# Performance work log

Hardware: AMD Instinct MI355X
Metric: run time of the kernel (lower is better)

## Reference

```python
import jax, jax.numpy as jnp
import numpy as np
import math

# ---- static configuration (matches init_kwargs) ----
B = 2
CIN, COUT = 128, 128
NLAT_IN, NLON_IN = 181, 360
NLAT_OUT, NLON_OUT = 181, 360
KSIZE = 3
PSCALE = NLON_IN // NLON_OUT  # longitude stride between output shifts
THETA_CUTOFF = KSIZE * math.pi / float(NLAT_IN - 1)


def _cc_weights(n):
    """Clenshaw-Curtis quadrature weights on [-1,1] for n equiangular nodes."""
    N = n - 1
    tk = np.pi * np.arange(n) / N
    j = np.arange(1, N // 2 + 1)
    b = np.where(2 * j == N, 1.0, 2.0)
    s = (b / (4.0 * j * j - 1.0)) @ np.cos(2.0 * np.outer(j, tk))
    w = (2.0 / N) * (1.0 - s)
    w[0] *= 0.5
    w[-1] *= 0.5
    return w[::-1].copy()  # flipped, as in _precompute_latitudes


def _lats(n):
    tk = np.pi * np.arange(n) / (n - 1)
    return tk[::-1].copy()  # lats = flip(arccos(cos(theta_k)))


def _precompute_psi():
    """Replicates _precompute_convolution_tensor + _compute_support_vals_isotropic.
    Returns COO entries (seg = k*NLAT_OUT + t, lat_in, lon_in, val)."""
    lats_in = _lats(NLAT_IN)
    lats_out = _lats(NLAT_OUT)
    phis = np.linspace(0.0, 2.0 * np.pi, NLON_IN)  # endpoint included (torch.linspace)
    dtheta = THETA_CUTOFF / KSIZE
    norm = 2.0 * np.pi * (1.0 - np.cos(THETA_CUTOFF))
    segs, lat_idx, lon_idx, vals = [], [], [], []
    alpha = lats_in[:, None]           # (nlat_in, 1)
    beta = phis[None, :]               # (1, nlon_in)
    for t in range(NLAT_OUT):
        gamma = lats_out[t]
        z = np.cos(alpha) * np.cos(gamma) - np.cos(beta) * np.sin(alpha) * np.sin(gamma)
        theta = np.arccos(np.clip(z, -1.0, 1.0))  # geodesic distance to rotated pole
        for k in range(KSIZE):
            d = np.abs(theta - k * dtheta)
            mask = (d <= dtheta) & (theta <= THETA_CUTOFF)
            ii, jj = np.nonzero(mask)
            if ii.size == 0:
                continue
            segs.append(np.full(ii.size, k * NLAT_OUT + t, dtype=np.int32))
            lat_idx.append(ii.astype(np.int32))
            lon_idx.append(jj.astype(np.int32))
            vals.append(((1.0 - d[ii, jj] / dtheta) / norm).astype(np.float32))
    return (np.concatenate(segs), np.concatenate(lat_idx),
            np.concatenate(lon_idx), np.concatenate(vals))


def setup_inputs() -> dict:
    key = jax.random.key(0)
    k1, k2, k3 = jax.random.split(key, 3)
    x = jax.random.normal(k1, (B, CIN, NLAT_IN, NLON_IN), dtype=jnp.float32)
    wgl = _cc_weights(NLAT_IN)
    quad_weights = jnp.asarray(2.0 * np.pi * wgl / NLON_IN, dtype=jnp.float32).reshape(-1, 1)
    seg, lat, lon, vals = _precompute_psi()
    weight = jax.random.normal(k2, (COUT, CIN, KSIZE), dtype=jnp.float32) / math.sqrt(CIN * KSIZE)
    bias = jax.random.normal(k3, (COUT,), dtype=jnp.float32) * 0.01
    return {"x": x, "quad_weights": quad_weights,
            "psi_vals": jnp.asarray(vals), "weight": weight, "bias": bias,
            "psi_seg": jnp.asarray(seg), "psi_lat": jnp.asarray(lat), "psi_lon": jnp.asarray(lon)}


def reference(x, quad_weights, psi_vals, weight, bias, psi_seg, psi_lat, psi_lon):
    Bb, C, H, W = x.shape
    # quadrature-weight the input, flatten spatial grid: (B*C, H*W)
    xw = (quad_weights * x).reshape(Bb * C, H * W)
    flat_base = psi_lat * W  # (nnz,)

    def step(carry, p):
        # shifted sparse contraction for output longitude p
        lon = (psi_lon + p * PSCALE) % W
        g = xw[:, flat_base + lon] * psi_vals[None, :]                 # (BC, nnz)
        yp = jax.ops.segment_sum(g.T, psi_seg, num_segments=KSIZE * NLAT_OUT)  # (K*T, BC)
        return carry, yp

    _, ys = jax.lax.scan(step, None, jnp.arange(NLON_OUT))            # (P, K*T, BC)
    y = ys.reshape(NLON_OUT, KSIZE, NLAT_OUT, Bb, C).transpose(3, 4, 1, 2, 0)  # (B,C,K,T,P)
    # grouped channel mixing (groups=1): 'bgckxy,fck->bfxy'
    out = jnp.einsum('bckxy,fck->bfxy', y, weight) + bias[None, :, None, None]
    return out
```

## Files before the change

kernel.cpp:

```cpp
#include <hip/hip_runtime.h>
#include <stdint.h>

#define HW     65160
#define W_LON  360
#define H_LAT  181
#define T_OUT  181
#define NB     2
#define NC     128
#define NF     128
#define NK     3
#define NSEG   (NK * T_OUT)
#define XROWS  65280
#define RW     720
#define LDSW   (7 * RW + 16)

typedef __attribute__((ext_vector_type(8))) short bf16x8;
typedef __attribute__((ext_vector_type(4))) float f32x4;
typedef __attribute__((ext_vector_type(2))) float f32x2;

#define AS1(p) ((const __attribute__((address_space(1))) void*)(p))
#define AS3(p) ((__attribute__((address_space(3))) void*)(p))

static __device__ inline ushort f2bf(float v) {
    unsigned u = __float_as_uint(v);
    unsigned r = (u + 0x7FFFu + ((u >> 16) & 1u)) >> 16;
    return (ushort)r;
}
static __device__ inline float bf2f(ushort h) {
    return __uint_as_float(((unsigned)h) << 16);
}


__global__ void k_transpose_w(const float* __restrict__ w,
                              ushort* __restrict__ wt_h, ushort* __restrict__ wt_l) {
    int i = blockIdx.x * 256 + threadIdx.x;
    if (i >= NK * NF * NC) return;
    int k = i / (NF * NC);
    int f = (i / NC) % NF;
    int c = i % NC;
    float v = w[(f * NC + c) * NK + k];
    ushort h = f2bf(v);
    ushort l = f2bf(v - bf2f(h));
    wt_h[i] = h;
    wt_l[i] = l;
}

__global__ void k_bounds(const int* __restrict__ seg, int* __restrict__ row_start,
                         int* __restrict__ row_end, int nnz) {
    int s = blockIdx.x * 256 + threadIdx.x;
    if (s >= NSEG) return;
    int t = s % T_OUT, k = s / T_OUT;
    int key = t * NK + k;
    int lo = 0, hi = nnz;
    while (lo < hi) {
        int mid = (lo + hi) >> 1;
        int sm = seg[mid];
        int km = (sm % T_OUT) * NK + sm / T_OUT;
        if (km < key) lo = mid + 1; else hi = mid;
    }
    row_start[s] = lo;
    int lo2 = lo; hi = nnz;
    while (lo2 < hi) {
        int mid = (lo2 + hi) >> 1;
        int sm = seg[mid];
        int km = (sm % T_OUT) * NK + sm / T_OUT;
        if (km <= key) lo2 = mid + 1; else hi = mid;
    }
    row_end[s] = lo2;
}

__global__ void k_pack(const int* __restrict__ seg, const int* __restrict__ lat,
                       const int* __restrict__ lon, const float* __restrict__ vals,
                       const float* __restrict__ qw,
                       uint2* __restrict__ packed, int nnz) {
    int n = blockIdx.x * 256 + threadIdx.x;
    if (n >= nnz) return;
    int s = seg[n];
    int k = s / T_OUT;
    int t = s - k * T_OUT;
    int la = lat[n];
    int dl = la - (t - 3);
    dl = max(0, min(6, dl));
    int lo = lon[n];
    unsigned ofs = (unsigned)(dl * RW + (lo & 1) * 360 + (lo >> 1));
    float v = vals[n] * qw[la];
    packed[n] = make_uint2(ofs, __float_as_uint(v));
}

__global__ __launch_bounds__(256) void k_split(const float* __restrict__ x,
                                               ushort* __restrict__ xt_h,
                                               ushort* __restrict__ xt_l) {
    int b = blockIdx.y;
    int hw0 = blockIdx.x * 64;
    __shared__ float t[128][65];
    int tid = threadIdx.x;
    int quad = tid & 15;
    int r0 = tid >> 4;
    bool full = (hw0 + 64 <= HW);
#pragma unroll
    for (int rr = 0; rr < 8; ++rr) {
        int c = rr * 16 + r0;
        const float* src = x + ((size_t)b * NC + c) * HW + hw0 + quad * 4;
        float4 v;
        if (full) {
            v = *(const float4*)src;
        } else {
            int base = hw0 + quad * 4;
            v.x = (base + 0 < HW) ? src[0] : 0.f;
            v.y = (base + 1 < HW) ? src[1] : 0.f;
            v.z = (base + 2 < HW) ? src[2] : 0.f;
            v.w = (base + 3 < HW) ? src[3] : 0.f;
        }
        *(float4*)&t[c][quad * 4] = v;
    }
    __syncthreads();
    int hwl = tid >> 2;
    int c0 = (tid & 3) * 32;
    int hw = hw0 + hwl;
    if (hw < HW) {
        ushort hb[32], lb[32];
#pragma unroll
        for (int cc = 0; cc < 32; ++cc) {
            float v = t[c0 + cc][hwl];
            ushort h = f2bf(v);
            hb[cc] = h;
            lb[cc] = f2bf(v - bf2f(h));
        }
        size_t off = ((size_t)b * XROWS + hw) * NC + c0;
#pragma unroll
        for (int j = 0; j < 4; ++j) {
            *(int4*)(xt_h + off + j * 8) = *(int4*)(hb + j * 8);
            *(int4*)(xt_l + off + j * 8) = *(int4*)(lb + j * 8);
        }
    }
}

template<int MT>
__global__ __launch_bounds__(256)
void k_gemm2(const ushort* __restrict__ xt_h, const ushort* __restrict__ xt_l,
             const ushort* __restrict__ wt_h,
             ushort* __restrict__ z, int cf0) {
    constexpr int MTILES = MT / 16;
    int tid = threadIdx.x;
    int bk = blockIdx.y;
    int b = bk / NK, k = bk % NK;
    int hwb = blockIdx.x * 256;

    __shared__ ushort smem[MT * 32 + 2 * 256 * 32];
    ushort* Ah = smem;
    ushort* Bh = smem + MT * 32;
    ushort* Bl = Bh + 256 * 32;

    int lane = tid & 63;
    int wv = tid >> 6;
    int m = lane & 15, q0 = lane >> 4;
    int eoff = (m * 4 + (q0 ^ ((m >> 1) & 3))) * 8;

    f32x4 acc[MTILES][4];
#pragma unroll
    for (int i = 0; i < MTILES; ++i)
#pragma unroll
        for (int j = 0; j < 4; ++j) acc[i][j] = (f32x4){0.f, 0.f, 0.f, 0.f};

    for (int c0 = 0; c0 < NC; c0 += 32) {
        if (tid < MT * 4) {
            int f = tid >> 2, s = tid & 3;
            int q = s ^ ((f >> 1) & 3);
            size_t gi = ((size_t)(k * NF + cf0 + f)) * NC + c0 + q * 8;
            int i0 = tid & ~63;
            __builtin_amdgcn_global_load_lds(AS1(wt_h + gi), AS3(Ah + i0 * 8), 16, 0, 0);
        }
#pragma unroll
        for (int it = 0; it < 4; ++it) {
            int i = it * 256 + tid;
            int r = i >> 2, s = i & 3;
            int q = s ^ ((r >> 1) & 3);
            size_t gi = ((size_t)b * XROWS + hwb + r) * NC + c0 + q * 8;
            int i0 = i & ~63;
            __builtin_amdgcn_global_load_lds(AS1(xt_h + gi), AS3(Bh + i0 * 8), 16, 0, 0);
            __builtin_amdgcn_global_load_lds(AS1(xt_l + gi), AS3(Bl + i0 * 8), 16, 0, 0);
        }
        __syncthreads();

        bf16x8 ah[MTILES], bh[4], bl[4];
#pragma unroll
        for (int mt = 0; mt < MTILES; ++mt)
            ah[mt] = *(const bf16x8*)(Ah + mt * 512 + eoff);
#pragma unroll
        for (int nt = 0; nt < 4; ++nt) {
            int boff = wv * 2048 + nt * 512 + eoff;
            bh[nt] = *(const bf16x8*)(Bh + boff);
            bl[nt] = *(const bf16x8*)(Bl + boff);
        }
#pragma unroll
        for (int mt = 0; mt < MTILES; ++mt)
#pragma unroll
            for (int nt = 0; nt < 4; ++nt) {
                acc[mt][nt] = __builtin_amdgcn_mfma_f32_16x16x32_bf16(ah[mt], bh[nt], acc[mt][nt], 0, 0, 0);
                acc[mt][nt] = __builtin_amdgcn_mfma_f32_16x16x32_bf16(ah[mt], bl[nt], acc[mt][nt], 0, 0, 0);
            }
        __syncthreads();
    }

#pragma unroll
    for (int mt = 0; mt < MTILES; ++mt)
#pragma unroll
        for (int nt = 0; nt < 4; ++nt) {
            int n = hwb + wv * 64 + nt * 16 + m;
            if (n < HW) {
                f32x4 a = acc[mt][nt];
#pragma unroll
                for (int r = 0; r < 4; ++r) {
                    int fl = mt * 16 + q0 * 4 + r;
                    z[((size_t)(b * NK + k) * MT + fl) * HW + n] = f2bf(a[r]);
                }
            }
        }
}

__global__ void __launch_bounds__(192)
k_sparse(const ushort* __restrict__ z, const uint2* __restrict__ packed,
         const int* __restrict__ row_start, const int* __restrict__ row_end,
         const float* __restrict__ bias,
         float* __restrict__ out, int cf0, int CF) {
    int y  = blockIdx.y;
    int t  = (y & 1) ? (T_OUT - 1 - (y >> 1)) : (y >> 1);
    int ch = blockIdx.x;
    int b  = ch / CF;
    int fl = ch % CF;
    int fg = cf0 + fl;
    int tid = threadIdx.x;
    __shared__ unsigned lds32[LDSW];

    int lat0 = t - 3;
    f32x2 acc = {0.f, 0.f};

    for (int k = 0; k < NK; ++k) {
        __syncthreads();
        const ushort* zplane = &z[(size_t)((b * NK + k) * CF + fl) * HW];
        for (int c = tid; c < 7 * 45; c += 192) {
            int r = c / 45, cj = (c - r * 45) * 4;
            int la = lat0 + r;
            if (la < 0 || la >= H_LAT) continue;
            const unsigned* g = (const unsigned*)(zplane + la * W_LON);
            uint4 a = *(const uint4*)(g + cj);
            unsigned nx = g[(cj + 4 < 180) ? cj + 4 : 0];
            uint4 bw;
            bw.x = (a.x >> 16) | (a.y << 16);
            bw.y = (a.y >> 16) | (a.z << 16);
            bw.z = (a.z >> 16) | (a.w << 16);
            bw.w = (a.w >> 16) | (nx << 16);
            unsigned* base = &lds32[r * RW + cj];
            *(uint4*)(base)       = a;
            *(uint4*)(base + 180) = a;
            *(uint4*)(base + 360) = bw;
            *(uint4*)(base + 540) = bw;
        }
        __syncthreads();

        int s = k * T_OUT + t;
        int ns = row_start[s], ne = row_end[s];
#pragma unroll 4
        for (int n = ns; n < ne; ++n) {
            uint2 e = packed[n];
            float v = __uint_as_float(e.y);
            unsigned u = lds32[(int)e.x + tid];
            f32x2 xv;
            xv[0] = __uint_as_float(u << 16);
            xv[1] = __uint_as_float(u & 0xFFFF0000u);
            f32x2 vv = {v, v};
#if __has_builtin(__builtin_elementwise_fma)
            acc = __builtin_elementwise_fma(vv, xv, acc);
#else
            acc[0] = fmaf(v, xv[0], acc[0]);
            acc[1] = fmaf(v, xv[1], acc[1]);
#endif
        }
    }

    if (tid < 180) {
        float bs = bias[fg];
        size_t ob = (size_t)((b * NF + fg) * T_OUT + t) * W_LON;
        float2 o = make_float2(acc[0] + bs, acc[1] + bs);
        *(float2*)&out[ob + 2 * tid] = o;
    }
}

extern "C" void kernel_launch(void* const* d_in, const int* in_sizes, int n_in,
                              void* d_out, int out_size, void* d_ws, size_t ws_size,
                              hipStream_t stream) {
    const float* x    = (const float*)d_in[0];
    const float* qw   = (const float*)d_in[1];
    const float* vals = (const float*)d_in[2];
    const float* w    = (const float*)d_in[3];
    const float* bias = (const float*)d_in[4];
    const int*   seg  = (const int*)d_in[5];
    const int*   lat  = (const int*)d_in[6];
    const int*   lon  = (const int*)d_in[7];
    int nnz = in_sizes[2];
    float* out = (float*)d_out;

    char* wsb = (char*)d_ws;
    ushort* wt_h     = (ushort*)wsb;
    ushort* wt_l     = (ushort*)(wsb + 98304);
    int*    row_start= (int*)(wsb + 196608);
    int*    row_end  = (int*)(wsb + 198912);
    uint2*  packed   = (uint2*)(wsb + 201216);
    size_t xoff = (201216 + (size_t)nnz * 8 + 255) & ~(size_t)255;
    size_t xtsz = (size_t)NB * XROWS * NC * 2;
    ushort* xt_h = (ushort*)(wsb + xoff);
    ushort* xt_l = (ushort*)(wsb + xoff + xtsz);
    size_t zoff = (xoff + 2 * xtsz + 255) & ~(size_t)255;
    ushort* z = (ushort*)(wsb + zoff);
    size_t zavail = (ws_size > zoff) ? ws_size - zoff : 0;

    int CF = 16;
    if      (zavail >= (size_t)64 * 6 * HW * 2) CF = 64;
    else if (zavail >= (size_t)32 * 6 * HW * 2) CF = 32;

    k_transpose_w<<<(NK * NF * NC + 255) / 256, 256, 0, stream>>>(w, wt_h, wt_l);
    k_pack<<<(nnz + 255) / 256, 256, 0, stream>>>(seg, lat, lon, vals, qw, packed, nnz);
    k_bounds<<<(NSEG + 255) / 256, 256, 0, stream>>>(seg, row_start, row_end, nnz);
    k_split<<<dim3((HW + 63) / 64, NB), 256, 0, stream>>>(x, xt_h, xt_l);

    int hwtiles = (HW + 255) / 256;
    for (int cf0 = 0; cf0 < NF; cf0 += CF) {
        dim3 gg(hwtiles, NB * NK);
        if (CF == 64)      k_gemm2<64><<<gg, 256, 0, stream>>>(xt_h, xt_l, wt_h, z, cf0);
        else if (CF == 32) k_gemm2<32><<<gg, 256, 0, stream>>>(xt_h, xt_l, wt_h, z, cf0);
        else               k_gemm2<16><<<gg, 256, 0, stream>>>(xt_h, xt_l, wt_h, z, cf0);
        dim3 gs(2 * CF, T_OUT);
        k_sparse<<<gs, 192, 0, stream>>>(z, packed, row_start, row_end, bias, out, cf0, CF);
    }
}
```

Measured before the change: 552.3 us.

## Split weights instead of activations, prefetch sparse planes, allow full-channel z buffer

The hi/lo bf16 split moves from the activation tensor to the weights, so k_split writes only one bf16 copy of x and the GEMM streams half as much activation data per tile, loading a small low-part weight tile instead. The sparse kernel now issues the global loads for the next k-plane before the gather loop and reuses precomputed row/column indices. The z buffer may hold all 128 output channels, so one sparse launch can follow several GEMM launches. The trade is lost precision from rounding x to bf16 and more workspace.

```diff
diff --git a/kernel.cpp b/kernel.cpp
--- a/kernel.cpp
+++ b/kernel.cpp
@@ -88,8 +88,7 @@
 }
 
 __global__ __launch_bounds__(256) void k_split(const float* __restrict__ x,
-                                               ushort* __restrict__ xt_h,
-                                               ushort* __restrict__ xt_l) {
+                                               ushort* __restrict__ xt_h) {
     int b = blockIdx.y;
     int hw0 = blockIdx.x * 64;
     __shared__ float t[128][65];
@@ -118,38 +117,32 @@
     int c0 = (tid & 3) * 32;
     int hw = hw0 + hwl;
     if (hw < HW) {
-        ushort hb[32], lb[32];
-#pragma unroll
-        for (int cc = 0; cc < 32; ++cc) {
-            float v = t[c0 + cc][hwl];
-            ushort h = f2bf(v);
-            hb[cc] = h;
-            lb[cc] = f2bf(v - bf2f(h));
-        }
+        ushort hb[32];
+#pragma unroll
+        for (int cc = 0; cc < 32; ++cc)
+            hb[cc] = f2bf(t[c0 + cc][hwl]);
         size_t off = ((size_t)b * XROWS + hw) * NC + c0;
 #pragma unroll
-        for (int j = 0; j < 4; ++j) {
+        for (int j = 0; j < 4; ++j)
             *(int4*)(xt_h + off + j * 8) = *(int4*)(hb + j * 8);
-            *(int4*)(xt_l + off + j * 8) = *(int4*)(lb + j * 8);
-        }
     }
 }
 
 template<int MT>
 __global__ __launch_bounds__(256)
-void k_gemm2(const ushort* __restrict__ xt_h, const ushort* __restrict__ xt_l,
-             const ushort* __restrict__ wt_h,
-             ushort* __restrict__ z, int cf0) {
+void k_gemm2(const ushort* __restrict__ xt_h,
+             const ushort* __restrict__ wt_h, const ushort* __restrict__ wt_l,
+             ushort* __restrict__ z, int cf0, int zcf, int zbase) {
     constexpr int MTILES = MT / 16;
     int tid = threadIdx.x;
     int bk = blockIdx.y;
     int b = bk / NK, k = bk % NK;
     int hwb = blockIdx.x * 256;
 
-    __shared__ ushort smem[MT * 32 + 2 * 256 * 32];
+    __shared__ ushort smem[2 * MT * 32 + 256 * 32];
     ushort* Ah = smem;
-    ushort* Bh = smem + MT * 32;
-    ushort* Bl = Bh + 256 * 32;
+    ushort* Al = smem + MT * 32;
+    ushort* Bh = smem + 2 * MT * 32;
 
     int lane = tid & 63;
     int wv = tid >> 6;
@@ -169,6 +162,7 @@
             size_t gi = ((size_t)(k * NF + cf0 + f)) * NC + c0 + q * 8;
             int i0 = tid & ~63;
             __builtin_amdgcn_global_load_lds(AS1(wt_h + gi), AS3(Ah + i0 * 8), 16, 0, 0);
+            __builtin_amdgcn_global_load_lds(AS1(wt_l + gi), AS3(Al + i0 * 8), 16, 0, 0);
         }
 #pragma unroll
         for (int it = 0; it < 4; ++it) {
@@ -178,26 +172,24 @@
             size_t gi = ((size_t)b * XROWS + hwb + r) * NC + c0 + q * 8;
             int i0 = i & ~63;
             __builtin_amdgcn_global_load_lds(AS1(xt_h + gi), AS3(Bh + i0 * 8), 16, 0, 0);
-            __builtin_amdgcn_global_load_lds(AS1(xt_l + gi), AS3(Bl + i0 * 8), 16, 0, 0);
         }
         __syncthreads();
 
-        bf16x8 ah[MTILES], bh[4], bl[4];
-#pragma unroll
-        for (int mt = 0; mt < MTILES; ++mt)
+        bf16x8 ah[MTILES], al[MTILES], bh[4];
+#pragma unroll
+        for (int mt = 0; mt < MTILES; ++mt) {
             ah[mt] = *(const bf16x8*)(Ah + mt * 512 + eoff);
-#pragma unroll
-        for (int nt = 0; nt < 4; ++nt) {
-            int boff = wv * 2048 + nt * 512 + eoff;
-            bh[nt] = *(const bf16x8*)(Bh + boff);
-            bl[nt] = *(const bf16x8*)(Bl + boff);
-        }
+            al[mt] = *(const bf16x8*)(Al + mt * 512 + eoff);
+        }
+#pragma unroll
+        for (int nt = 0; nt < 4; ++nt)
+            bh[nt] = *(const bf16x8*)(Bh + wv * 2048 + nt * 512 + eoff);
 #pragma unroll
         for (int mt = 0; mt < MTILES; ++mt)
 #pragma unroll
             for (int nt = 0; nt < 4; ++nt) {
                 acc[mt][nt] = __builtin_amdgcn_mfma_f32_16x16x32_bf16(ah[mt], bh[nt], acc[mt][nt], 0, 0, 0);
-                acc[mt][nt] = __builtin_amdgcn_mfma_f32_16x16x32_bf16(ah[mt], bl[nt], acc[mt][nt], 0, 0, 0);
+                acc[mt][nt] = __builtin_amdgcn_mfma_f32_16x16x32_bf16(al[mt], bh[nt], acc[mt][nt], 0, 0, 0);
             }
         __syncthreads();
     }
@@ -212,7 +204,7 @@
 #pragma unroll
                 for (int r = 0; r < 4; ++r) {
                     int fl = mt * 16 + q0 * 4 + r;
-                    z[((size_t)(b * NK + k) * MT + fl) * HW + n] = f2bf(a[r]);
+                    z[((size_t)(b * NK + k) * zcf + zbase + fl) * HW + n] = f2bf(a[r]);
                 }
             }
         }
@@ -235,28 +227,59 @@
     int lat0 = t - 3;
     f32x2 acc = {0.f, 0.f};
 
+    int c0s = tid,        r0s = c0s / 45, cj0 = (c0s - r0s * 45) * 4, la0 = lat0 + r0s;
+    int c1s = tid + 192;
+    int r1s = c1s / 45,   cj1 = (c1s - r1s * 45) * 4, la1 = lat0 + r1s;
+    bool v0 = (la0 >= 0 && la0 < H_LAT);
+    bool v1 = (c1s < 315) && (la1 >= 0 && la1 < H_LAT);
+    const size_t zpstride = (size_t)CF * HW;
+    const ushort* zb = &z[(size_t)(b * NK) * zpstride + (size_t)fl * HW];
+
+    uint4 a0, a1; unsigned n0 = 0, n1 = 0;
+    a0 = (uint4){0,0,0,0}; a1 = (uint4){0,0,0,0};
+
+    {
+        const unsigned* g0 = (const unsigned*)(zb + la0 * W_LON);
+        const unsigned* g1 = (const unsigned*)(zb + la1 * W_LON);
+        if (v0) { a0 = *(const uint4*)(g0 + cj0); n0 = g0[(cj0 + 4 < 180) ? cj0 + 4 : 0]; }
+        if (v1) { a1 = *(const uint4*)(g1 + cj1); n1 = g1[(cj1 + 4 < 180) ? cj1 + 4 : 0]; }
+    }
+
     for (int k = 0; k < NK; ++k) {
         __syncthreads();
-        const ushort* zplane = &z[(size_t)((b * NK + k) * CF + fl) * HW];
-        for (int c = tid; c < 7 * 45; c += 192) {
-            int r = c / 45, cj = (c - r * 45) * 4;
-            int la = lat0 + r;
-            if (la < 0 || la >= H_LAT) continue;
-            const unsigned* g = (const unsigned*)(zplane + la * W_LON);
-            uint4 a = *(const uint4*)(g + cj);
-            unsigned nx = g[(cj + 4 < 180) ? cj + 4 : 0];
+        if (v0) {
             uint4 bw;
-            bw.x = (a.x >> 16) | (a.y << 16);
-            bw.y = (a.y >> 16) | (a.z << 16);
-            bw.z = (a.z >> 16) | (a.w << 16);
-            bw.w = (a.w >> 16) | (nx << 16);
-            unsigned* base = &lds32[r * RW + cj];
-            *(uint4*)(base)       = a;
-            *(uint4*)(base + 180) = a;
+            bw.x = (a0.x >> 16) | (a0.y << 16);
+            bw.y = (a0.y >> 16) | (a0.z << 16);
+            bw.z = (a0.z >> 16) | (a0.w << 16);
+            bw.w = (a0.w >> 16) | (n0 << 16);
+            unsigned* base = &lds32[r0s * RW + cj0];
+            *(uint4*)(base)       = a0;
+            *(uint4*)(base + 180) = a0;
             *(uint4*)(base + 360) = bw;
             *(uint4*)(base + 540) = bw;
         }
+        if (v1) {
+            uint4 bw;
+            bw.x = (a1.x >> 16) | (a1.y << 16);
+            bw.y = (a1.y >> 16) | (a1.z << 16);
+            bw.z = (a1.z >> 16) | (a1.w << 16);
+            bw.w = (a1.w >> 16) | (n1 << 16);
+            unsigned* base = &lds32[r1s * RW + cj1];
+            *(uint4*)(base)       = a1;
+            *(uint4*)(base + 180) = a1;
+            *(uint4*)(base + 360) = bw;
+            *(uint4*)(base + 540) = bw;
+        }
         __syncthreads();
+
+        if (k + 1 < NK) {
+            const ushort* zp = zb + (size_t)(k + 1) * zpstride;
+            const unsigned* g0 = (const unsigned*)(zp + la0 * W_LON);
+            const unsigned* g1 = (const unsigned*)(zp + la1 * W_LON);
+            if (v0) { a0 = *(const uint4*)(g0 + cj0); n0 = g0[(cj0 + 4 < 180) ? cj0 + 4 : 0]; }
+            if (v1) { a1 = *(const uint4*)(g1 + cj1); n1 = g1[(cj1 + 4 < 180) ? cj1 + 4 : 0]; }
+        }
 
         int s = k * T_OUT + t;
         int ns = row_start[s], ne = row_end[s];
@@ -309,27 +332,30 @@
     size_t xoff = (201216 + (size_t)nnz * 8 + 255) & ~(size_t)255;
     size_t xtsz = (size_t)NB * XROWS * NC * 2;
     ushort* xt_h = (ushort*)(wsb + xoff);
-    ushort* xt_l = (ushort*)(wsb + xoff + xtsz);
-    size_t zoff = (xoff + 2 * xtsz + 255) & ~(size_t)255;
+    size_t zoff = (xoff + xtsz + 255) & ~(size_t)255;
     ushort* z = (ushort*)(wsb + zoff);
     size_t zavail = (ws_size > zoff) ? ws_size - zoff : 0;
 
     int CF = 16;
-    if      (zavail >= (size_t)64 * 6 * HW * 2) CF = 64;
-    else if (zavail >= (size_t)32 * 6 * HW * 2) CF = 32;
+    if      (zavail >= (size_t)128 * 6 * HW * 2) CF = 128;
+    else if (zavail >= (size_t)64 * 6 * HW * 2)  CF = 64;
+    else if (zavail >= (size_t)32 * 6 * HW * 2)  CF = 32;
 
     k_transpose_w<<<(NK * NF * NC + 255) / 256, 256, 0, stream>>>(w, wt_h, wt_l);
     k_pack<<<(nnz + 255) / 256, 256, 0, stream>>>(seg, lat, lon, vals, qw, packed, nnz);
     k_bounds<<<(NSEG + 255) / 256, 256, 0, stream>>>(seg, row_start, row_end, nnz);
-    k_split<<<dim3((HW + 63) / 64, NB), 256, 0, stream>>>(x, xt_h, xt_l);
+    k_split<<<dim3((HW + 63) / 64, NB), 256, 0, stream>>>(x, xt_h);
 
     int hwtiles = (HW + 255) / 256;
-    for (int cf0 = 0; cf0 < NF; cf0 += CF) {
-        dim3 gg(hwtiles, NB * NK);
-        if (CF == 64)      k_gemm2<64><<<gg, 256, 0, stream>>>(xt_h, xt_l, wt_h, z, cf0);
-        else if (CF == 32) k_gemm2<32><<<gg, 256, 0, stream>>>(xt_h, xt_l, wt_h, z, cf0);
-        else               k_gemm2<16><<<gg, 256, 0, stream>>>(xt_h, xt_l, wt_h, z, cf0);
+    int mt = (CF < 64) ? CF : 64;
+    for (int zf0 = 0; zf0 < NF; zf0 += CF) {
+        for (int cf0 = zf0; cf0 < zf0 + CF; cf0 += mt) {
+            dim3 gg(hwtiles, NB * NK);
+            if (mt == 64)      k_gemm2<64><<<gg, 256, 0, stream>>>(xt_h, wt_h, wt_l, z, cf0, CF, cf0 - zf0);
+            else if (mt == 32) k_gemm2<32><<<gg, 256, 0, stream>>>(xt_h, wt_h, wt_l, z, cf0, CF, cf0 - zf0);
+            else               k_gemm2<16><<<gg, 256, 0, stream>>>(xt_h, wt_h, wt_l, z, cf0, CF, cf0 - zf0);
+        }
         dim3 gs(2 * CF, T_OUT);
-        k_sparse<<<gs, 192, 0, stream>>>(z, packed, row_start, row_end, bias, out, cf0, CF);
-    }
-}
+        k_sparse<<<gs, 192, 0, stream>>>(z, packed, row_start, row_end, bias, out, zf0, CF);
+    }
+}
```

New measurement: 471.1 us. -14.7%, faster.
